# Performance work log

Hardware: AMD Instinct MI355X
Metric: run time of the kernel (lower is better)

## Reference

```python
import jax, jax.numpy as jnp
import numpy as np

FEATURES = 512
SPLIT_TT = 2
DK = FEATURES // SPLIT_TT           # 256: key width = features // split_tt
NUM_TAPE = 2048                     # ac_config.num_tape_tokens
THRESHOLD = 4.0                     # ac_config.dynamic_tape_length.act_epsilon
TOPK = int(NUM_TAPE // THRESHOLD)   # 512
TOKENS_PER_STEP = 16                # num_token_per_step
BATCH = 64


def setup_inputs() -> dict:
    key = jax.random.key(0)
    kq, kt = jax.random.split(key)
    return {
        "query": jax.random.normal(kq, (BATCH, DK), jnp.float32),
        "halting_prob": jnp.zeros((BATCH,), jnp.float32),
        "remainders": jnp.zeros((BATCH,), jnp.float32),
        "n_updates": jnp.zeros((BATCH,), jnp.float32),
        "score_mask": jnp.zeros((BATCH, NUM_TAPE), jnp.float32),
        "tape_tokens": jax.random.normal(kt, (BATCH, NUM_TAPE, FEATURES), jnp.float32),
    }


def reference(query, halting_prob, remainders, n_updates, score_mask, tape_tokens):
    # One ACT step (take_a_step / act_step) with bank_type='input',
    # act_loss_type='entropy', complex_query=True.
    still_running = (halting_prob < THRESHOLD).astype(jnp.float32)   # [B]

    # keys are the first DK features of the per-example tape bank
    keys = tape_tokens[:, :, :DK]                                    # [B, N, DK]
    scores = jnp.einsum('bd,bnd->bn', query, keys)                   # [B, N]

    # mask already-selected tokens, then top-k
    topk_idx = jax.lax.top_k(scores - score_mask * 1e9, TOPK)[1]     # [B, K] int32

    # NOTE: faithful to original: jnp.take without axis => FLAT gather into
    # scores.ravel(); indices in [0, N) all address row 0 of scores.
    weights = jnp.take(scores, topk_idx)                             # [B, K]
    weights = jax.nn.softmax(weights / (query.shape[-1] ** 0.5), axis=-1)

    entropy = 1.0 - jnp.sum(weights ** 2, axis=-1)                   # [B]
    sum_weights = jnp.sum(weights[:, :TOKENS_PER_STEP], axis=-1)     # [B]

    new_halted = (halting_prob + sum_weights >= THRESHOLD).astype(jnp.float32) * still_running
    still_running = still_running - new_halted
    remainders = remainders + (new_halted + still_running) * entropy
    halting_prob = halting_prob + sum_weights * still_running
    halting_prob = halting_prob + new_halted * (THRESHOLD - halting_prob)
    n_updates = n_updates + still_running + new_halted

    # gather selected tape tokens per example, softmax-weighted merge
    token_sel = jnp.take_along_axis(tape_tokens, topk_idx[..., None], axis=1)  # [B, K, F]
    token_sel = jnp.sum(token_sel * weights[..., None], axis=-2, keepdims=True)  # [B, 1, F]

    # scatter-accumulate selection mask
    score_mask = score_mask + jnp.sum(jax.nn.one_hot(topk_idx, NUM_TAPE), axis=1)  # [B, N]

    # complex_query update
    token_sel_keys = token_sel[:, :, :DK]                            # [B, 1, DK]
    query = (query + jnp.mean(token_sel_keys, axis=1)) / 2.0         # [B, DK]

    return (query, halting_prob, remainders, n_updates, score_mask, token_sel)
```

## Files before the change

### kernel.cpp

```cpp
#include <hip/hip_runtime.h>
#include <math.h>

#define BATCH 64
#define DK 256
#define FEATURES 512
#define NUM_TAPE 2048
#define TOPK 512
#define TOP16 16
#define THRESH 4.0f
#define KCHUNKS 8
#define KPER (TOPK / KCHUNKS)
#define TIECAP 640

#define OFF_Q 0
#define OFF_HP (BATCH * DK)
#define OFF_REM (OFF_HP + BATCH)
#define OFF_NUP (OFF_REM + BATCH)
#define OFF_MASK (OFF_NUP + BATCH)
#define OFF_TSEL (OFF_MASK + BATCH * NUM_TAPE)

#define WS_SCORES 0
#define WS_TOPK 131072
#define WS_WEIGHTS 163840
#define WS_PART 196608

__device__ __forceinline__ unsigned f2key(float f) {
    unsigned u = __float_as_uint(f);
    return (u & 0x80000000u) ? ~u : (u | 0x80000000u);
}

__global__ __launch_bounds__(256) void k_scores(const float* __restrict__ q,
                                                const float* __restrict__ tape,
                                                float* __restrict__ scores) {
    const int b = blockIdx.y;
    const int wave = threadIdx.x >> 6;
    const int lane = threadIdx.x & 63;
    const float4 qf = reinterpret_cast<const float4*>(q + b * DK)[lane];
    const int base = blockIdx.x * 32;
#pragma unroll
    for (int t = 0; t < 8; ++t) {
        const int tok = base + wave + 4 * t;
        const float4 tf =
            reinterpret_cast<const float4*>(tape + ((size_t)b * NUM_TAPE + tok) * FEATURES)[lane];
        float s = qf.x * tf.x + qf.y * tf.y + qf.z * tf.z + qf.w * tf.w;
#pragma unroll
        for (int off = 32; off; off >>= 1) s += __shfl_xor(s, off);
        if (lane == 0) scores[b * NUM_TAPE + tok] = s;
    }
}

__global__ __launch_bounds__(512) void k_topk(const float* __restrict__ scores,
                                              const float* __restrict__ mask_in,
                                              const float* __restrict__ hp_in,
                                              const float* __restrict__ rem_in,
                                              const float* __restrict__ nup_in,
                                              int* __restrict__ topk_ws,
                                              float* __restrict__ weights_ws,
                                              float* __restrict__ out) {
    const int b = blockIdx.x;
    const int tid = threadIdx.x;
    const int lane = tid & 63;
    const int wv = tid >> 6;
    __shared__ int hist[256];
    __shared__ int chunkTot[4];
    __shared__ int sh_digit, sh_hi;
    __shared__ int sel_idx[TOPK];
    __shared__ unsigned sel_key[TOPK];
    __shared__ float redf[8];
    __shared__ int tie_idx[TIECAP];
    __shared__ int tie_cnt, sel_cnt;
    __shared__ int in16_idx[TOP16];

    const float4 sc = reinterpret_cast<const float4*>(scores + (size_t)b * NUM_TAPE)[tid];
    const float4 mk = reinterpret_cast<const float4*>(mask_in + (size_t)b * NUM_TAPE)[tid];
    unsigned key[4];
    key[0] = f2key(sc.x - mk.x * 1e9f);
    key[1] = f2key(sc.y - mk.y * 1e9f);
    key[2] = f2key(sc.z - mk.z * 1e9f);
    key[3] = f2key(sc.w - mk.w * 1e9f);

    unsigned prefix = 0;
    int krem = TOPK;
#pragma unroll
    for (int p = 0; p < 4; ++p) {
        const int shift = 24 - 8 * p;
        if (tid < 256) hist[tid] = 0;
        __syncthreads();
#pragma unroll
        for (int i = 0; i < 4; ++i) {
            const unsigned kk = key[i];
            const bool act = (p == 0) || ((kk >> (shift + 8)) == (prefix >> (shift + 8)));
            if (act) atomicAdd(&hist[(kk >> shift) & 0xFF], 1);
        }
        __syncthreads();
        int v = 0, hcnt = 0;
        if (tid < 256) {
            hcnt = hist[tid];
            v = hcnt;
#pragma unroll
            for (int off = 1; off < 64; off <<= 1) {
                const int t = __shfl_down(v, off);
                if (lane + off < 64) v += t;
            }
            if (lane == 0) chunkTot[wv] = v;
        }
        __syncthreads();
        if (tid < 256) {
#pragma unroll
            for (int w2 = 0; w2 < 4; ++w2)
                if (w2 > wv) v += chunkTot[w2];
            if (v >= krem && (v - hcnt) < krem) {
                sh_digit = tid;
                sh_hi = v - hcnt;
            }
        }
        __syncthreads();
        prefix |= ((unsigned)sh_digit) << shift;
        krem -= sh_hi;
        __syncthreads();
    }
    const unsigned T512 = prefix;
    const int krem512 = krem;

    if (tid == 0) {
        sel_cnt = 0;
        tie_cnt = 0;
    }
    __syncthreads();
#pragma unroll
    for (int i = 0; i < 4; ++i) {
        const int e = 4 * tid + i;
        const unsigned kk = key[i];
        if (kk > T512) {
            const int p = atomicAdd(&sel_cnt, 1);
            sel_idx[p] = e;
            sel_key[p] = kk;
        } else if (kk == T512) {
            const int p = atomicAdd(&tie_cnt, 1);
            if (p < TIECAP) tie_idx[p] = e;
        }
    }
    __syncthreads();
    int tc = tie_cnt < TIECAP ? tie_cnt : TIECAP;
    for (int t = tid; t < tc; t += 512) {
        const int my = tie_idx[t];
        int rank = 0;
        for (int u = 0; u < tc; ++u) rank += (tie_idx[u] < my);
        if (rank < krem512) {
            const int p = atomicAdd(&sel_cnt, 1);
            sel_idx[p] = my;
            sel_key[p] = T512;
        }
    }
    __syncthreads();

    const unsigned kk2 = sel_key[tid];
    prefix = 0;
    krem = TOP16;
#pragma unroll
    for (int p = 0; p < 4; ++p) {
        const int shift = 24 - 8 * p;
        if (tid < 256) hist[tid] = 0;
        __syncthreads();
        {
            const bool act = (p == 0) || ((kk2 >> (shift + 8)) == (prefix >> (shift + 8)));
            if (act) atomicAdd(&hist[(kk2 >> shift) & 0xFF], 1);
        }
        __syncthreads();
        int v = 0, hcnt = 0;
        if (tid < 256) {
            hcnt = hist[tid];
            v = hcnt;
#pragma unroll
            for (int off = 1; off < 64; off <<= 1) {
                const int t = __shfl_down(v, off);
                if (lane + off < 64) v += t;
            }
            if (lane == 0) chunkTot[wv] = v;
        }
        __syncthreads();
        if (tid < 256) {
#pragma unroll
            for (int w2 = 0; w2 < 4; ++w2)
                if (w2 > wv) v += chunkTot[w2];
            if (v >= krem && (v - hcnt) < krem) {
                sh_digit = tid;
                sh_hi = v - hcnt;
            }
        }
        __syncthreads();
        prefix |= ((unsigned)sh_digit) << shift;
        krem -= sh_hi;
        __syncthreads();
    }
    const unsigned T16 = prefix;
    const int krem16 = krem;

    if (tid == 0) tie_cnt = 0;
    __syncthreads();
    if (kk2 == T16) {
        const int p = atomicAdd(&tie_cnt, 1);
        if (p < TIECAP) tie_idx[p] = sel_idx[tid];
    }
    __syncthreads();
    tc = tie_cnt < TIECAP ? tie_cnt : TIECAP;
    for (int t = tid; t < tc; t += 512) {
        const int my = tie_idx[t];
        int rank = 0;
        for (int u = 0; u < tc; ++u) rank += (tie_idx[u] < my);
        if (rank < krem16) in16_idx[rank] = my;
    }
    __syncthreads();

    const int myidx = sel_idx[tid];
    const float wraw = scores[myidx] * 0.0625f;

    float m = wraw;
#pragma unroll
    for (int off = 32; off; off >>= 1) m = fmaxf(m, __shfl_xor(m, off));
    if (lane == 0) redf[wv] = m;
    __syncthreads();
#pragma unroll
    for (int w2 = 0; w2 < 8; ++w2) m = fmaxf(m, redf[w2]);
    __syncthreads();

    const float e = expf(wraw - m);
    float s = e;
#pragma unroll
    for (int off = 32; off; off >>= 1) s += __shfl_xor(s, off);
    if (lane == 0) redf[wv] = s;
    __syncthreads();
    s = 0.f;
#pragma unroll
    for (int w2 = 0; w2 < 8; ++w2) s += redf[w2];
    __syncthreads();

    const float w = e / s;
    weights_ws[b * TOPK + tid] = w;
    topk_ws[b * TOPK + tid] = myidx;

    float lsq = w * w;
#pragma unroll
    for (int off = 32; off; off >>= 1) lsq += __shfl_xor(lsq, off);
    if (lane == 0) redf[wv] = lsq;
    __syncthreads();
    float sumsq = 0.f;
#pragma unroll
    for (int w2 = 0; w2 < 8; ++w2) sumsq += redf[w2];
    __syncthreads();

    bool in16 = (kk2 > T16);
    if (kk2 == T16) {
        for (int u = 0; u < krem16; ++u)
            if (in16_idx[u] == myidx) in16 = true;
    }
    float l16 = in16 ? w : 0.f;
#pragma unroll
    for (int off = 32; off; off >>= 1) l16 += __shfl_xor(l16, off);
    if (lane == 0) redf[wv] = l16;
    __syncthreads();
    float s16 = 0.f;
#pragma unroll
    for (int w2 = 0; w2 < 8; ++w2) s16 += redf[w2];

    if (tid == 0) {
        const float hp = hp_in[b], rem = rem_in[b], nup = nup_in[b];
        const float entropy = 1.0f - sumsq;
        const float still = (hp < THRESH) ? 1.f : 0.f;
        const float nh = ((hp + s16) >= THRESH ? 1.f : 0.f) * still;
        const float st2 = still - nh;
        out[OFF_REM + b] = rem + (nh + st2) * entropy;
        float hp1 = hp + s16 * st2;
        hp1 = hp1 + nh * (THRESH - hp1);
        out[OFF_HP + b] = hp1;
        out[OFF_NUP + b] = nup + st2 + nh;
    }

    reinterpret_cast<float4*>(out + OFF_MASK + (size_t)b * NUM_TAPE)[tid] = mk;
    __syncthreads();
    out[OFF_MASK + b * NUM_TAPE + myidx] = mask_in[b * NUM_TAPE + myidx] + 1.0f;
}

__global__ __launch_bounds__(512) void k_gather(const float* __restrict__ tape,
                                                const int* __restrict__ topk_ws,
                                                const float* __restrict__ weights_ws,
                                                float* __restrict__ partials) {
    const int b = blockIdx.y;
    const int kc = blockIdx.x;
    const int rs = threadIdx.x >> 7;
    const int f4 = threadIdx.x & 127;
    __shared__ float wsh[KPER];
    __shared__ int ish[KPER];
    __shared__ float4 shacc[512];
    if (threadIdx.x < KPER) {
        wsh[threadIdx.x] = weights_ws[b * TOPK + kc * KPER + threadIdx.x];
        ish[threadIdx.x] = topk_ws[b * TOPK + kc * KPER + threadIdx.x];
    }
    __syncthreads();
    float4 acc = {0.f, 0.f, 0.f, 0.f};
#pragma unroll 4
    for (int k = rs; k < KPER; k += 4) {
        const float w = wsh[k];
        const float4 t =
            reinterpret_cast<const float4*>(tape + ((size_t)b * NUM_TAPE + ish[k]) * FEATURES)[f4];
        acc.x = fmaf(w, t.x, acc.x);
        acc.y = fmaf(w, t.y, acc.y);
        acc.z = fmaf(w, t.z, acc.z);
        acc.w = fmaf(w, t.w, acc.w);
    }
    shacc[threadIdx.x] = acc;
    __syncthreads();
    if (threadIdx.x < 128) {
        const float4 a0 = shacc[f4];
        const float4 a1 = shacc[128 + f4];
        const float4 a2 = shacc[256 + f4];
        const float4 a3 = shacc[384 + f4];
        float4 r;
        r.x = (a0.x + a1.x) + (a2.x + a3.x);
        r.y = (a0.y + a1.y) + (a2.y + a3.y);
        r.z = (a0.z + a1.z) + (a2.z + a3.z);
        r.w = (a0.w + a1.w) + (a2.w + a3.w);
        reinterpret_cast<float4*>(partials + ((size_t)b * KCHUNKS + kc) * FEATURES)[f4] = r;
    }
}

__global__ __launch_bounds__(512) void k_finish(const float* __restrict__ q,
                                                const float* __restrict__ partials,
                                                float* __restrict__ out) {
    const int b = blockIdx.x;
    const int g = threadIdx.x >> 7;
    const int f4 = threadIdx.x & 127;
    __shared__ float4 sh[512];
    const float4* pp = reinterpret_cast<const float4*>(partials + (size_t)b * KCHUNKS * FEATURES);
    const float4 a = pp[g * 128 + f4];
    const float4 c = pp[(g + 4) * 128 + f4];
    float4 r;
    r.x = a.x + c.x;
    r.y = a.y + c.y;
    r.z = a.z + c.z;
    r.w = a.w + c.w;
    sh[threadIdx.x] = r;
    __syncthreads();
    if (threadIdx.x < 128) {
        const float4 s0 = sh[f4];
        const float4 s1 = sh[128 + f4];
        const float4 s2 = sh[256 + f4];
        const float4 s3 = sh[384 + f4];
        float4 s;
        s.x = (s0.x + s1.x) + (s2.x + s3.x);
        s.y = (s0.y + s1.y) + (s2.y + s3.y);
        s.z = (s0.z + s1.z) + (s2.z + s3.z);
        s.w = (s0.w + s1.w) + (s2.w + s3.w);
        reinterpret_cast<float4*>(out + OFF_TSEL + (size_t)b * FEATURES)[f4] = s;
        if (f4 < 64) {
            const float4 qv = reinterpret_cast<const float4*>(q + (size_t)b * DK)[f4];
            float4 nq;
            nq.x = (qv.x + s.x) * 0.5f;
            nq.y = (qv.y + s.y) * 0.5f;
            nq.z = (qv.z + s.z) * 0.5f;
            nq.w = (qv.w + s.w) * 0.5f;
            reinterpret_cast<float4*>(out + OFF_Q + (size_t)b * DK)[f4] = nq;
        }
    }
}

extern "C" void kernel_launch(void* const* d_in, const int* in_sizes, int n_in,
                              void* d_out, int out_size, void* d_ws, size_t ws_size,
                              hipStream_t stream) {
    const float* q = (const float*)d_in[0];
    const float* hp = (const float*)d_in[1];
    const float* rem = (const float*)d_in[2];
    const float* nup = (const float*)d_in[3];
    const float* mask = (const float*)d_in[4];
    const float* tape = (const float*)d_in[5];
    float* out = (float*)d_out;
    float* ws = (float*)d_ws;

    float* scores = ws + WS_SCORES;
    int* topk = (int*)(ws + WS_TOPK);
    float* weights = ws + WS_WEIGHTS;
    float* partials = ws + WS_PART;

    k_scores<<<dim3(NUM_TAPE / 32, BATCH), 256, 0, stream>>>(q, tape, scores);
    k_topk<<<BATCH, 512, 0, stream>>>(scores, mask, hp, rem, nup, topk, weights, out);
    k_gather<<<dim3(KCHUNKS, BATCH), 512, 0, stream>>>(tape, topk, weights, partials);
    k_finish<<<BATCH, 512, 0, stream>>>(q, partials, out);
}
```

Before: 50.73 us.

## Fuse top-k selection into gather kernel with redundant per-chunk selection

Merges the top-k and gather kernels into one launch. Each of the 8 chunk blocks per batch row redoes the selection and then gathers the selected tokens whose tape index falls in its own 256-token range. The radix select drops from four 8-bit passes to two, followed by a pairwise ranking of the remaining candidates. This removes one kernel launch and the round trip of indices and weights through workspace. In exchange, every chunk block repeats the full selection work, which is 8x redundant compute, and the gather per block now handles an uneven number of tokens.

```diff
diff --git a/kernel.cpp b/kernel.cpp
--- a/kernel.cpp
+++ b/kernel.cpp
@@ -9,8 +9,8 @@
 #define TOP16 16
 #define THRESH 4.0f
 #define KCHUNKS 8
-#define KPER (TOPK / KCHUNKS)
-#define TIECAP 640
+#define RANGE (NUM_TAPE / KCHUNKS)
+#define CAP 640
 
 #define OFF_Q 0
 #define OFF_HP (BATCH * DK)
@@ -20,13 +20,58 @@
 #define OFF_TSEL (OFF_MASK + BATCH * NUM_TAPE)
 
 #define WS_SCORES 0
-#define WS_TOPK 131072
-#define WS_WEIGHTS 163840
-#define WS_PART 196608
+#define WS_PART 131072
 
 __device__ __forceinline__ unsigned f2key(float f) {
     unsigned u = __float_as_uint(f);
     return (u & 0x80000000u) ? ~u : (u | 0x80000000u);
+}
+
+#define RADIX_FIND(KREM)                                              \
+    {                                                                 \
+        int v = 0, hcnt = 0;                                          \
+        if (tid < 256) {                                              \
+            hcnt = hist[tid];                                         \
+            v = hcnt;                                                 \
+            _Pragma("unroll") for (int off = 1; off < 64; off <<= 1) {\
+                const int t = __shfl_down(v, off);                    \
+                if (lane + off < 64) v += t;                          \
+            }                                                         \
+            if (lane == 0) chunkTot[wv] = v;                          \
+        }                                                             \
+        __syncthreads();                                              \
+        if (tid < 256) {                                              \
+            _Pragma("unroll") for (int w2 = 0; w2 < 4; ++w2)          \
+                if (w2 > wv) v += chunkTot[w2];                       \
+            if (v >= (KREM) && (v - hcnt) < (KREM)) {                 \
+                sh_digit = tid;                                       \
+                sh_hi = v - hcnt;                                     \
+            }                                                         \
+        }                                                             \
+        __syncthreads();                                              \
+    }
+
+__device__ __forceinline__ float block_max8(float v, volatile float* redf, int lane, int wv) {
+#pragma unroll
+    for (int off = 32; off; off >>= 1) v = fmaxf(v, __shfl_xor(v, off));
+    if (lane == 0) redf[wv] = v;
+    __syncthreads();
+#pragma unroll
+    for (int w2 = 0; w2 < 8; ++w2) v = fmaxf(v, redf[w2]);
+    __syncthreads();
+    return v;
+}
+
+__device__ __forceinline__ float block_sum8(float v, volatile float* redf, int lane, int wv) {
+#pragma unroll
+    for (int off = 32; off; off >>= 1) v += __shfl_xor(v, off);
+    if (lane == 0) redf[wv] = v;
+    __syncthreads();
+    float s = 0.f;
+#pragma unroll
+    for (int w2 = 0; w2 < 8; ++w2) s += redf[w2];
+    __syncthreads();
+    return s;
 }
 
 __global__ __launch_bounds__(256) void k_scores(const float* __restrict__ q,
@@ -49,268 +94,228 @@
     }
 }
 
-__global__ __launch_bounds__(512) void k_topk(const float* __restrict__ scores,
-                                              const float* __restrict__ mask_in,
-                                              const float* __restrict__ hp_in,
-                                              const float* __restrict__ rem_in,
-                                              const float* __restrict__ nup_in,
-                                              int* __restrict__ topk_ws,
-                                              float* __restrict__ weights_ws,
-                                              float* __restrict__ out) {
-    const int b = blockIdx.x;
+__global__ __launch_bounds__(512) void k_select_gather(
+    const float* __restrict__ scores, const float* __restrict__ mask_in,
+    const float* __restrict__ hp_in, const float* __restrict__ rem_in,
+    const float* __restrict__ nup_in, const float* __restrict__ tape,
+    float* __restrict__ partials, float* __restrict__ out) {
+    const int b = blockIdx.y;
+    const int kc = blockIdx.x;
     const int tid = threadIdx.x;
     const int lane = tid & 63;
     const int wv = tid >> 6;
+
     __shared__ int hist[256];
     __shared__ int chunkTot[4];
     __shared__ int sh_digit, sh_hi;
-    __shared__ int sel_idx[TOPK];
-    __shared__ unsigned sel_key[TOPK];
+    __shared__ unsigned ckey[CAP];
+    __shared__ int cidx[CAP];
+    __shared__ int csel[CAP];
+    __shared__ int cand_n;
     __shared__ float redf[8];
-    __shared__ int tie_idx[TIECAP];
-    __shared__ int tie_cnt, sel_cnt;
-    __shared__ int in16_idx[TOP16];
+    __shared__ int gl_idx[RANGE];
+    __shared__ float gl_w[RANGE];
+    __shared__ int gl_n;
+    __shared__ float4 shacc[512];
 
     const float4 sc = reinterpret_cast<const float4*>(scores + (size_t)b * NUM_TAPE)[tid];
     const float4 mk = reinterpret_cast<const float4*>(mask_in + (size_t)b * NUM_TAPE)[tid];
+    const float4 s0 = reinterpret_cast<const float4*>(scores)[tid];
     unsigned key[4];
     key[0] = f2key(sc.x - mk.x * 1e9f);
     key[1] = f2key(sc.y - mk.y * 1e9f);
     key[2] = f2key(sc.z - mk.z * 1e9f);
     key[3] = f2key(sc.w - mk.w * 1e9f);
-
-    unsigned prefix = 0;
-    int krem = TOPK;
-#pragma unroll
-    for (int p = 0; p < 4; ++p) {
-        const int shift = 24 - 8 * p;
-        if (tid < 256) hist[tid] = 0;
-        __syncthreads();
-#pragma unroll
-        for (int i = 0; i < 4; ++i) {
-            const unsigned kk = key[i];
-            const bool act = (p == 0) || ((kk >> (shift + 8)) == (prefix >> (shift + 8)));
-            if (act) atomicAdd(&hist[(kk >> shift) & 0xFF], 1);
-        }
-        __syncthreads();
-        int v = 0, hcnt = 0;
-        if (tid < 256) {
-            hcnt = hist[tid];
-            v = hcnt;
-#pragma unroll
-            for (int off = 1; off < 64; off <<= 1) {
-                const int t = __shfl_down(v, off);
-                if (lane + off < 64) v += t;
+    float s0v[4] = {s0.x * 0.0625f, s0.y * 0.0625f, s0.z * 0.0625f, s0.w * 0.0625f};
+    float mkv[4] = {mk.x, mk.y, mk.z, mk.w};
+
+    if (tid < 256) hist[tid] = 0;
+    __syncthreads();
+#pragma unroll
+    for (int j = 0; j < 4; ++j) atomicAdd(&hist[key[j] >> 24], 1);
+    __syncthreads();
+    RADIX_FIND(TOPK);
+    const unsigned B1 = (unsigned)sh_digit;
+    const int above1 = sh_hi;
+    __syncthreads();
+
+    if (tid < 256) hist[tid] = 0;
+    __syncthreads();
+#pragma unroll
+    for (int j = 0; j < 4; ++j)
+        if ((key[j] >> 24) == B1) atomicAdd(&hist[(key[j] >> 16) & 0xFF], 1);
+    __syncthreads();
+    const int kremB = TOPK - above1;
+    RADIX_FIND(kremB);
+    const unsigned P16 = (B1 << 8) | (unsigned)sh_digit;
+    const int krem512 = kremB - sh_hi;
+    __syncthreads();
+
+    if (tid == 0) cand_n = 0;
+    __syncthreads();
+    int cpos[4];
+#pragma unroll
+    for (int j = 0; j < 4; ++j) {
+        cpos[j] = -1;
+        if ((key[j] >> 16) == P16) {
+            const int p = atomicAdd(&cand_n, 1);
+            if (p < CAP) {
+                ckey[p] = key[j];
+                cidx[p] = 4 * tid + j;
             }
-            if (lane == 0) chunkTot[wv] = v;
-        }
-        __syncthreads();
-        if (tid < 256) {
-#pragma unroll
-            for (int w2 = 0; w2 < 4; ++w2)
-                if (w2 > wv) v += chunkTot[w2];
-            if (v >= krem && (v - hcnt) < krem) {
-                sh_digit = tid;
-                sh_hi = v - hcnt;
+            cpos[j] = p;
+        }
+    }
+    __syncthreads();
+    int cn = cand_n < CAP ? cand_n : CAP;
+    for (int t = tid; t < cn; t += 512) {
+        const unsigned k = ckey[t];
+        const int i = cidx[t];
+        int r = 0;
+        for (int u = 0; u < cn; ++u) {
+            const unsigned ko = ckey[u];
+            r += (ko > k) || (ko == k && cidx[u] < i);
+        }
+        csel[t] = (r < krem512);
+    }
+    __syncthreads();
+    bool sel[4];
+#pragma unroll
+    for (int j = 0; j < 4; ++j)
+        sel[j] = ((key[j] >> 16) > P16) ||
+                 (cpos[j] >= 0 && cpos[j] < CAP && csel[cpos[j]]);
+    __syncthreads();
+
+    if (tid < 256) hist[tid] = 0;
+    __syncthreads();
+#pragma unroll
+    for (int j = 0; j < 4; ++j)
+        if (sel[j]) atomicAdd(&hist[key[j] >> 24], 1);
+    __syncthreads();
+    RADIX_FIND(TOP16);
+    const unsigned C1 = (unsigned)sh_digit;
+    const int krem16 = TOP16 - sh_hi;
+    __syncthreads();
+
+    if (tid == 0) cand_n = 0;
+    __syncthreads();
+    int c2pos[4];
+#pragma unroll
+    for (int j = 0; j < 4; ++j) {
+        c2pos[j] = -1;
+        if (sel[j] && (key[j] >> 24) == C1) {
+            const int p = atomicAdd(&cand_n, 1);
+            if (p < CAP) {
+                ckey[p] = key[j];
+                cidx[p] = 4 * tid + j;
             }
-        }
-        __syncthreads();
-        prefix |= ((unsigned)sh_digit) << shift;
-        krem -= sh_hi;
-        __syncthreads();
-    }
-    const unsigned T512 = prefix;
-    const int krem512 = krem;
-
-    if (tid == 0) {
-        sel_cnt = 0;
-        tie_cnt = 0;
-    }
-    __syncthreads();
-#pragma unroll
-    for (int i = 0; i < 4; ++i) {
-        const int e = 4 * tid + i;
-        const unsigned kk = key[i];
-        if (kk > T512) {
-            const int p = atomicAdd(&sel_cnt, 1);
-            sel_idx[p] = e;
-            sel_key[p] = kk;
-        } else if (kk == T512) {
-            const int p = atomicAdd(&tie_cnt, 1);
-            if (p < TIECAP) tie_idx[p] = e;
-        }
-    }
-    __syncthreads();
-    int tc = tie_cnt < TIECAP ? tie_cnt : TIECAP;
-    for (int t = tid; t < tc; t += 512) {
-        const int my = tie_idx[t];
-        int rank = 0;
-        for (int u = 0; u < tc; ++u) rank += (tie_idx[u] < my);
-        if (rank < krem512) {
-            const int p = atomicAdd(&sel_cnt, 1);
-            sel_idx[p] = my;
-            sel_key[p] = T512;
-        }
-    }
-    __syncthreads();
-
-    const unsigned kk2 = sel_key[tid];
-    prefix = 0;
-    krem = TOP16;
-#pragma unroll
-    for (int p = 0; p < 4; ++p) {
-        const int shift = 24 - 8 * p;
-        if (tid < 256) hist[tid] = 0;
-        __syncthreads();
-        {
-            const bool act = (p == 0) || ((kk2 >> (shift + 8)) == (prefix >> (shift + 8)));
-            if (act) atomicAdd(&hist[(kk2 >> shift) & 0xFF], 1);
-        }
-        __syncthreads();
-        int v = 0, hcnt = 0;
-        if (tid < 256) {
-            hcnt = hist[tid];
-            v = hcnt;
-#pragma unroll
-            for (int off = 1; off < 64; off <<= 1) {
-                const int t = __shfl_down(v, off);
-                if (lane + off < 64) v += t;
+            c2pos[j] = p;
+        }
+    }
+    __syncthreads();
+    cn = cand_n < CAP ? cand_n : CAP;
+    for (int t = tid; t < cn; t += 512) {
+        const unsigned k = ckey[t];
+        const int i = cidx[t];
+        int r = 0;
+        for (int u = 0; u < cn; ++u) {
+            const unsigned ko = ckey[u];
+            r += (ko > k) || (ko == k && cidx[u] < i);
+        }
+        csel[t] = (r < krem16);
+    }
+    __syncthreads();
+    bool in16[4];
+#pragma unroll
+    for (int j = 0; j < 4; ++j)
+        in16[j] = sel[j] && (((key[j] >> 24) > C1) ||
+                             (c2pos[j] >= 0 && c2pos[j] < CAP && csel[c2pos[j]]));
+
+    float mloc = -3e38f;
+#pragma unroll
+    for (int j = 0; j < 4; ++j)
+        if (sel[j]) mloc = fmaxf(mloc, s0v[j]);
+    const float m = block_max8(mloc, redf, lane, wv);
+
+    float ev[4];
+    float eloc = 0.f;
+#pragma unroll
+    for (int j = 0; j < 4; ++j) {
+        ev[j] = sel[j] ? expf(s0v[j] - m) : 0.f;
+        eloc += ev[j];
+    }
+    const float ssum = block_sum8(eloc, redf, lane, wv);
+    const float inv = 1.0f / ssum;
+
+    float w[4];
+    float lsq = 0.f, l16 = 0.f;
+#pragma unroll
+    for (int j = 0; j < 4; ++j) {
+        w[j] = ev[j] * inv;
+        lsq += w[j] * w[j];
+        if (in16[j]) l16 += w[j];
+    }
+    const float sumsq = block_sum8(lsq, redf, lane, wv);
+    const float s16 = block_sum8(l16, redf, lane, wv);
+
+    if (kc == 0) {
+        float4 om;
+        om.x = mkv[0] + (sel[0] ? 1.f : 0.f);
+        om.y = mkv[1] + (sel[1] ? 1.f : 0.f);
+        om.z = mkv[2] + (sel[2] ? 1.f : 0.f);
+        om.w = mkv[3] + (sel[3] ? 1.f : 0.f);
+        reinterpret_cast<float4*>(out + OFF_MASK + (size_t)b * NUM_TAPE)[tid] = om;
+        if (tid == 0) {
+            const float hp = hp_in[b], rem = rem_in[b], nup = nup_in[b];
+            const float entropy = 1.0f - sumsq;
+            const float still = (hp < THRESH) ? 1.f : 0.f;
+            const float nh = ((hp + s16) >= THRESH ? 1.f : 0.f) * still;
+            const float st2 = still - nh;
+            out[OFF_REM + b] = rem + (nh + st2) * entropy;
+            float hp1 = hp + s16 * st2;
+            hp1 = hp1 + nh * (THRESH - hp1);
+            out[OFF_HP + b] = hp1;
+            out[OFF_NUP + b] = nup + st2 + nh;
+        }
+    }
+
+    if (wv == kc) {
+        const int cnt = (sel[0] ? 1 : 0) + (sel[1] ? 1 : 0) + (sel[2] ? 1 : 0) + (sel[3] ? 1 : 0);
+        int pre = cnt;
+#pragma unroll
+        for (int off = 1; off < 64; off <<= 1) {
+            const int t = __shfl_up(pre, off);
+            if (lane >= off) pre += t;
+        }
+        int p = pre - cnt;
+#pragma unroll
+        for (int j = 0; j < 4; ++j) {
+            if (sel[j]) {
+                gl_idx[p] = 4 * tid + j;
+                gl_w[p] = w[j];
+                ++p;
             }
-            if (lane == 0) chunkTot[wv] = v;
-        }
-        __syncthreads();
-        if (tid < 256) {
-#pragma unroll
-            for (int w2 = 0; w2 < 4; ++w2)
-                if (w2 > wv) v += chunkTot[w2];
-            if (v >= krem && (v - hcnt) < krem) {
-                sh_digit = tid;
-                sh_hi = v - hcnt;
-            }
-        }
-        __syncthreads();
-        prefix |= ((unsigned)sh_digit) << shift;
-        krem -= sh_hi;
-        __syncthreads();
-    }
-    const unsigned T16 = prefix;
-    const int krem16 = krem;
-
-    if (tid == 0) tie_cnt = 0;
-    __syncthreads();
-    if (kk2 == T16) {
-        const int p = atomicAdd(&tie_cnt, 1);
-        if (p < TIECAP) tie_idx[p] = sel_idx[tid];
-    }
-    __syncthreads();
-    tc = tie_cnt < TIECAP ? tie_cnt : TIECAP;
-    for (int t = tid; t < tc; t += 512) {
-        const int my = tie_idx[t];
-        int rank = 0;
-        for (int u = 0; u < tc; ++u) rank += (tie_idx[u] < my);
-        if (rank < krem16) in16_idx[rank] = my;
-    }
-    __syncthreads();
-
-    const int myidx = sel_idx[tid];
-    const float wraw = scores[myidx] * 0.0625f;
-
-    float m = wraw;
-#pragma unroll
-    for (int off = 32; off; off >>= 1) m = fmaxf(m, __shfl_xor(m, off));
-    if (lane == 0) redf[wv] = m;
-    __syncthreads();
-#pragma unroll
-    for (int w2 = 0; w2 < 8; ++w2) m = fmaxf(m, redf[w2]);
-    __syncthreads();
-
-    const float e = expf(wraw - m);
-    float s = e;
-#pragma unroll
-    for (int off = 32; off; off >>= 1) s += __shfl_xor(s, off);
-    if (lane == 0) redf[wv] = s;
-    __syncthreads();
-    s = 0.f;
-#pragma unroll
-    for (int w2 = 0; w2 < 8; ++w2) s += redf[w2];
-    __syncthreads();
-
-    const float w = e / s;
-    weights_ws[b * TOPK + tid] = w;
-    topk_ws[b * TOPK + tid] = myidx;
-
-    float lsq = w * w;
-#pragma unroll
-    for (int off = 32; off; off >>= 1) lsq += __shfl_xor(lsq, off);
-    if (lane == 0) redf[wv] = lsq;
-    __syncthreads();
-    float sumsq = 0.f;
-#pragma unroll
-    for (int w2 = 0; w2 < 8; ++w2) sumsq += redf[w2];
-    __syncthreads();
-
-    bool in16 = (kk2 > T16);
-    if (kk2 == T16) {
-        for (int u = 0; u < krem16; ++u)
-            if (in16_idx[u] == myidx) in16 = true;
-    }
-    float l16 = in16 ? w : 0.f;
-#pragma unroll
-    for (int off = 32; off; off >>= 1) l16 += __shfl_xor(l16, off);
-    if (lane == 0) redf[wv] = l16;
-    __syncthreads();
-    float s16 = 0.f;
-#pragma unroll
-    for (int w2 = 0; w2 < 8; ++w2) s16 += redf[w2];
-
-    if (tid == 0) {
-        const float hp = hp_in[b], rem = rem_in[b], nup = nup_in[b];
-        const float entropy = 1.0f - sumsq;
-        const float still = (hp < THRESH) ? 1.f : 0.f;
-        const float nh = ((hp + s16) >= THRESH ? 1.f : 0.f) * still;
-        const float st2 = still - nh;
-        out[OFF_REM + b] = rem + (nh + st2) * entropy;
-        float hp1 = hp + s16 * st2;
-        hp1 = hp1 + nh * (THRESH - hp1);
-        out[OFF_HP + b] = hp1;
-        out[OFF_NUP + b] = nup + st2 + nh;
-    }
-
-    reinterpret_cast<float4*>(out + OFF_MASK + (size_t)b * NUM_TAPE)[tid] = mk;
-    __syncthreads();
-    out[OFF_MASK + b * NUM_TAPE + myidx] = mask_in[b * NUM_TAPE + myidx] + 1.0f;
-}
-
-__global__ __launch_bounds__(512) void k_gather(const float* __restrict__ tape,
-                                                const int* __restrict__ topk_ws,
-                                                const float* __restrict__ weights_ws,
-                                                float* __restrict__ partials) {
-    const int b = blockIdx.y;
-    const int kc = blockIdx.x;
-    const int rs = threadIdx.x >> 7;
-    const int f4 = threadIdx.x & 127;
-    __shared__ float wsh[KPER];
-    __shared__ int ish[KPER];
-    __shared__ float4 shacc[512];
-    if (threadIdx.x < KPER) {
-        wsh[threadIdx.x] = weights_ws[b * TOPK + kc * KPER + threadIdx.x];
-        ish[threadIdx.x] = topk_ws[b * TOPK + kc * KPER + threadIdx.x];
-    }
-    __syncthreads();
+        }
+        if (lane == 63) gl_n = pre;
+    }
+    __syncthreads();
+    const int nsel = gl_n;
+
+    const int rs = tid >> 7;
+    const int f4 = tid & 127;
     float4 acc = {0.f, 0.f, 0.f, 0.f};
-#pragma unroll 4
-    for (int k = rs; k < KPER; k += 4) {
-        const float w = wsh[k];
+    for (int k = rs; k < nsel; k += 4) {
+        const float ww = gl_w[k];
         const float4 t =
-            reinterpret_cast<const float4*>(tape + ((size_t)b * NUM_TAPE + ish[k]) * FEATURES)[f4];
-        acc.x = fmaf(w, t.x, acc.x);
-        acc.y = fmaf(w, t.y, acc.y);
-        acc.z = fmaf(w, t.z, acc.z);
-        acc.w = fmaf(w, t.w, acc.w);
-    }
-    shacc[threadIdx.x] = acc;
-    __syncthreads();
-    if (threadIdx.x < 128) {
+            reinterpret_cast<const float4*>(tape + ((size_t)b * NUM_TAPE + gl_idx[k]) * FEATURES)[f4];
+        acc.x = fmaf(ww, t.x, acc.x);
+        acc.y = fmaf(ww, t.y, acc.y);
+        acc.z = fmaf(ww, t.z, acc.z);
+        acc.w = fmaf(ww, t.w, acc.w);
+    }
+    shacc[tid] = acc;
+    __syncthreads();
+    if (tid < 128) {
         const float4 a0 = shacc[f4];
         const float4 a1 = shacc[128 + f4];
         const float4 a2 = shacc[256 + f4];
@@ -377,12 +382,10 @@
     float* ws = (float*)d_ws;
 
     float* scores = ws + WS_SCORES;
-    int* topk = (int*)(ws + WS_TOPK);
-    float* weights = ws + WS_WEIGHTS;
     float* partials = ws + WS_PART;
 
     k_scores<<<dim3(NUM_TAPE / 32, BATCH), 256, 0, stream>>>(q, tape, scores);
-    k_topk<<<BATCH, 512, 0, stream>>>(scores, mask, hp, rem, nup, topk, weights, out);
-    k_gather<<<dim3(KCHUNKS, BATCH), 512, 0, stream>>>(tape, topk, weights, partials);
+    k_select_gather<<<dim3(KCHUNKS, BATCH), 512, 0, stream>>>(
+        scores, mask, hp, rem, nup, tape, partials, out);
     k_finish<<<BATCH, 512, 0, stream>>>(q, partials, out);
 }
```

After: 53.90 us. 6.2% more time.
